# Kernel optimization log

Hardware: AMD Instinct MI355X
Metric: run time of the kernel (lower is better)

## Reference

```python
import jax, jax.numpy as jnp
from jax import lax
import numpy as np

B, N, C = 4, 2048, 64          # batch, num points, feature channels
M = 512                         # num centroids (FPS)
SAMPLES = (32, 64)              # neighbors per scale
RADII = (0.2, 0.4)              # ball radii per scale
MLPS = ((67, 64, 64, 128), (67, 128, 128, 256))  # in->hidden->out per scale (in = C + 3)


def setup_inputs() -> dict:
    key = jax.random.key(0)
    ks = jax.random.split(key, 16)
    inp = {
        "points": jax.random.uniform(ks[0], (B, 3, N), jnp.float32),   # unit cube
        "features": jax.random.normal(ks[1], (B, C, N), jnp.float32),
    }
    k = 2
    for s, dims in enumerate(MLPS):
        for l in range(3):
            cin, cout = dims[l], dims[l + 1]
            inp[f"w{s}_{l}"] = (jax.random.normal(ks[k], (cout, cin), jnp.float32)
                                * jnp.float32(1.0 / np.sqrt(cin)))
            inp[f"b{s}_{l}"] = jnp.zeros((cout,), jnp.float32)
            k += 1
    return inp


def fps(xyz, m):
    """Farthest point sampling. xyz: (B,N,3) -> indices (B,m) int32."""
    b, n, _ = xyz.shape
    big = jnp.asarray(1e10, xyz.dtype)

    def step(carry, _):
        dist, cur = carry                                   # (B,N), (B,)
        cur_pt = jnp.take_along_axis(xyz, cur[:, None, None], axis=1)  # (B,1,3)
        d2 = jnp.sum((xyz - cur_pt) ** 2, axis=-1)          # (B,N)
        dist = jnp.minimum(dist, d2)
        nxt = jnp.argmax(dist, axis=-1).astype(jnp.int32)
        return (dist, nxt), cur

    init = (jnp.full((b, n), big, xyz.dtype), jnp.zeros((b,), jnp.int32))
    _, idxs = lax.scan(step, init, None, length=m)          # (m,B)
    return idxs.T                                           # (B,m)


def ball_group(xyz, feat_t, cent, s, r):
    """Ball query + group gather. Returns (B,M,s,3+C) = [rel_xyz; features]."""
    n = xyz.shape[1]
    d2 = jnp.sum((cent[:, :, None, :] - xyz[:, None, :, :]) ** 2, axis=-1)  # (B,M,N)
    keys = jnp.where(d2 <= r * r, jnp.arange(n, dtype=jnp.int32), n)
    idx = jnp.sort(keys, axis=-1)[:, :, :s]                 # first s in-ball indices
    idx = jnp.where(idx < n, idx, idx[:, :, :1])            # pad with first valid
    gxyz = jax.vmap(lambda p, i: p[i])(xyz, idx) - cent[:, :, None, :]  # (B,M,s,3)
    gfeat = jax.vmap(lambda f, i: f[i])(feat_t, idx)        # (B,M,s,C)
    return jnp.concatenate([gxyz, gfeat], axis=-1)


def mlp_max(g, ws, bs):
    """Shared 1x1-conv MLP over (B,M,S,Cin), max over neighbor dim S."""
    x = g
    for w, b in zip(ws, bs):
        x = jax.nn.relu(jnp.einsum('bmsc,oc->bmso', x, w) + b)
    return jnp.max(x, axis=2)                               # (B,M,Cout)


def reference(points, features,
              w0_0, b0_0, w0_1, b0_1, w0_2, b0_2,
              w1_0, b1_0, w1_1, b1_1, w1_2, b1_2):
    xyz = jnp.transpose(points, (0, 2, 1))                  # (B,N,3)
    feat_t = jnp.transpose(features, (0, 2, 1))             # (B,N,C)
    idx = fps(xyz, M)                                       # (B,M)
    cent = jnp.take_along_axis(xyz, idx[:, :, None], axis=1)  # (B,M,3)
    Ws = [(w0_0, w0_1, w0_2), (w1_0, w1_1, w1_2)]
    Bs = [(b0_0, b0_1, b0_2), (b1_0, b1_1, b1_2)]
    outs = []
    for i, (s, r) in enumerate(zip(SAMPLES, RADII)):
        g = ball_group(xyz, feat_t, cent, s, r)             # (B,M,s,3+C)
        outs.append(mlp_max(g, Ws[i], Bs[i]))               # (B,M,Cout_i)
    feat = jnp.transpose(jnp.concatenate(outs, axis=-1), (0, 2, 1))  # (B,384,M)
    return jnp.transpose(cent, (0, 2, 1)), feat             # (B,3,M), (B,384,M)
```

## Files before the change

kernel.cpp:

```cpp
#include <hip/hip_runtime.h>

#define NPTS 2048
#define BATCH 4
#define CFEAT 64
#define MCENT 512

typedef float f4 __attribute__((ext_vector_type(4)));
typedef float f2 __attribute__((ext_vector_type(2)));
typedef short s8v __attribute__((ext_vector_type(8)));

__device__ __forceinline__ unsigned short f2bf(float x) {
    unsigned u = __float_as_uint(x);
    return (unsigned short)((u + 0x7fffu + ((u >> 16) & 1u)) >> 16);
}

template <int CTRL>
__device__ __forceinline__ float dpp_max_step(float v) {
    int t = __builtin_amdgcn_update_dpp(0, __float_as_int(v), CTRL, 0xf, 0xf, true);
    return fmaxf(v, __int_as_float(t));
}

__device__ __forceinline__ float readlane_f(float v, int l) {
    return __int_as_float(__builtin_amdgcn_readlane(__float_as_int(v), l));
}

template <int COUT, int CIN, int KPW, bool PERM>
__device__ void pack_seg(const float* w, unsigned short* dst, int start, int stride) {
    for (int i = start; i < COUT * KPW; i += stride) {
        int o = i / KPW, k = i - o * KPW;
        float v = 0.f;
        if (PERM) {
            if (k < 64) v = w[o * CIN + 3 + k];
            else if (k < 67) v = w[o * CIN + (k - 64)];
        } else {
            if (k < CIN) v = w[o * CIN + k];
        }
        dst[i] = f2bf(v);
    }
}

__global__ __launch_bounds__(256, 1) void fps_prep(
    const float* __restrict__ pts, const float* __restrict__ feats,
    const float* w00, const float* w01, const float* w02,
    const float* w10, const float* w11, const float* w12,
    float* cent, unsigned short* ftr, unsigned short* wp, float* out)
{
    const int tid = threadIdx.x;
    if (blockIdx.x >= 4) {
        const int stride = 64 * 256;
        const int start = (blockIdx.x - 4) * 256 + tid;
        for (int i = start; i < BATCH * NPTS * CFEAT; i += stride) {
            int c = i & 63, n = (i >> 6) & (NPTS - 1), b = i >> 17;
            ftr[i] = f2bf(feats[(b * CFEAT + c) * NPTS + n]);
        }
        pack_seg<64, 67, 96, true>(w00, wp + 0, start, stride);
        pack_seg<64, 64, 64, false>(w01, wp + 6144, start, stride);
        pack_seg<128, 64, 64, false>(w02, wp + 10240, start, stride);
        pack_seg<128, 67, 96, true>(w10, wp + 18432, start, stride);
        pack_seg<128, 128, 128, false>(w11, wp + 30720, start, stride);
        pack_seg<256, 128, 128, false>(w12, wp + 47104, start, stride);
        return;
    }
    const int b = blockIdx.x;
    const int lane = tid & 63, wv = tid >> 6;
    const float* px = pts + b * 3 * NPTS;
    const float* py = px + NPTS;
    const float* pz = py + NPTS;
    __shared__ __align__(16) float4 slotq[8 * 2];
    __shared__ __align__(16) float4 scent[MCENT];

    __builtin_amdgcn_s_setprio(3);

    const int base = wv * 512 + lane * 8;
    f2 rx[4], ry[4], rz[4], rd[4];
#pragma unroll
    for (int i = 0; i < 4; ++i) {
        rx[i] = *(const f2*)(px + base + 2 * i);
        ry[i] = *(const f2*)(py + base + 2 * i);
        rz[i] = *(const f2*)(pz + base + 2 * i);
        rd[i] = (f2){1e10f, 1e10f};
    }
    float cx = px[0], cy = py[0], cz = pz[0];
    int par = 0;
    for (int m = 0; m < MCENT; ++m) {
        if (tid == 0) scent[m] = make_float4(cx, cy, cz, 0.f);
        {
#pragma clang fp contract(off)
            f2 c2x = {cx, cx}, c2y = {cy, cy}, c2z = {cz, cz};
#pragma unroll
            for (int i = 0; i < 4; ++i) {
                f2 dx = rx[i] - c2x, dy = ry[i] - c2y, dz = rz[i] - c2z;
                f2 d2 = dx * dx + dy * dy;
                d2 = d2 + dz * dz;
                f2 old = rd[i];
                f2 nd;
                nd.x = fminf(old.x, d2.x);
                nd.y = fminf(old.y, d2.y);
                rd[i] = nd;
            }
        }
        float n0 = rd[0].x, n1 = rd[0].y, n2 = rd[1].x, n3 = rd[1].y;
        float n4 = rd[2].x, n5 = rd[2].y, n6 = rd[3].x, n7 = rd[3].y;
        float bv = fmaxf(fmaxf(fmaxf(n0, n1), fmaxf(n2, n3)),
                         fmaxf(fmaxf(n4, n5), fmaxf(n6, n7)));
        float ox = rx[3].y, oy = ry[3].y, oz = rz[3].y;
        {
            float ndv[8] = {n0, n1, n2, n3, n4, n5, n6, n7};
#pragma unroll
            for (int k = 6; k >= 0; --k) {
                bool t = (ndv[k] == bv);
                float nx = (k & 1) ? rx[k >> 1].y : rx[k >> 1].x;
                float ny = (k & 1) ? ry[k >> 1].y : ry[k >> 1].x;
                float nz = (k & 1) ? rz[k >> 1].y : rz[k >> 1].x;
                ox = t ? nx : ox; oy = t ? ny : oy; oz = t ? nz : oz;
            }
        }
        float v = bv;
        v = dpp_max_step<0x111>(v);
        v = dpp_max_step<0x112>(v);
        v = dpp_max_step<0x114>(v);
        v = dpp_max_step<0x118>(v);
        v = dpp_max_step<0x142>(v);
        v = dpp_max_step<0x143>(v);
        float wmax = readlane_f(v, 63);
        unsigned long long cand = __ballot(bv == wmax);
        int wl = __ffsll(cand) - 1;
        if (lane == wl) slotq[(par * 4 + wv) * 2] = make_float4(bv, ox, oy, oz);
        __syncthreads();
        float4 s0 = slotq[(par * 4 + 0) * 2];
        float4 s1 = slotq[(par * 4 + 1) * 2];
        float4 s2 = slotq[(par * 4 + 2) * 2];
        float4 s3 = slotq[(par * 4 + 3) * 2];
        float4 c01 = (s1.x > s0.x) ? s1 : s0;
        float4 c23 = (s3.x > s2.x) ? s3 : s2;
        float4 cc  = (c23.x > c01.x) ? c23 : c01;
        cx = cc.y; cy = cc.z; cz = cc.w;
        par ^= 1;
    }
    __syncthreads();
    float* outc = out + b * 3 * MCENT;
    for (int m = tid; m < MCENT; m += 256) {
        float4 c = scent[m];
        float* cw = cent + (b * MCENT + m) * 3;
        cw[0] = c.x; cw[1] = c.y; cw[2] = c.z;
        outc[m] = c.x; outc[MCENT + m] = c.y; outc[2 * MCENT + m] = c.z;
    }
}

template <int MT, int KSTEPS, int NTW>
__device__ __forceinline__ void layer_mm(const unsigned short* A, const unsigned short* __restrict__ Wg,
                                         const float* __restrict__ bias, int lane, int wv,
                                         f4 (&acc)[MT][NTW])
{
    constexpr int KP = KSTEPS * 32;
    const int r15 = lane & 15, g = lane >> 4;
#pragma unroll
    for (int nt = 0; nt < NTW; ++nt) {
        int n = (wv * NTW + nt) * 16 + r15;
        float bv = bias[n];
#pragma unroll
        for (int mt = 0; mt < MT; ++mt) acc[mt][nt] = (f4){bv, bv, bv, bv};
    }
#pragma unroll
    for (int ks = 0; ks < KSTEPS; ++ks) {
        s8v afr[MT];
#pragma unroll
        for (int mt = 0; mt < MT; ++mt) {
            int row = mt * 16 + r15;
            int byte = ((row * KP + ks * 32 + g * 8) * 2) ^ ((row & 7) << 4);
            afr[mt] = *(const s8v*)((const char*)A + byte);
        }
#pragma unroll
        for (int nt = 0; nt < NTW; ++nt) {
            int n = (wv * NTW + nt) * 16 + r15;
            s8v bfr = *(const s8v*)(Wg + n * KP + ks * 32 + g * 8);
#pragma unroll
            for (int mt = 0; mt < MT; ++mt)
                acc[mt][nt] = __builtin_amdgcn_mfma_f32_16x16x32_bf16(afr[mt], bfr, acc[mt][nt], 0, 0, 0);
        }
    }
}

template <int MT, int NTW, int CO>
__device__ __forceinline__ void store_lds(f4 (&acc)[MT][NTW], unsigned short* OUT, int lane, int wv) {
    const int r15 = lane & 15, g = lane >> 4;
#pragma unroll
    for (int mt = 0; mt < MT; ++mt)
#pragma unroll
        for (int nt = 0; nt < NTW; ++nt)
#pragma unroll
            for (int q = 0; q < 4; ++q) {
                int j = mt * 16 + g * 4 + q;
                int n = (wv * NTW + nt) * 16 + r15;
                float v = fmaxf(acc[mt][nt][q], 0.f);
                int byte = ((j * CO + n) * 2) ^ ((j & 7) << 4);
                *(unsigned short*)((char*)OUT + byte) = f2bf(v);
            }
}

template <int S_, int C1, int C2, int C3>
__device__ __forceinline__ void msg_body(int bm, char* smem,
    const float* __restrict__ pts, const unsigned short* __restrict__ ftr,
    const float* __restrict__ cent,
    const unsigned short* __restrict__ W0, const float* __restrict__ B0,
    const unsigned short* __restrict__ W1, const float* __restrict__ B1,
    const unsigned short* __restrict__ W2, const float* __restrict__ B2,
    float* __restrict__ outf, int ch_off, float rr)
{
    constexpr int MT = S_ / 16;
    constexpr int KS1 = C1 / 32, KS2 = C2 / 32;
    constexpr int NW1 = C1 / 64, NW2 = C2 / 64, NW3 = C3 / 64;
    constexpr int HA = (S_ * 96 > S_ * C2) ? S_ * 96 : S_ * C2;
    unsigned short* hA = (unsigned short*)smem;
    unsigned short* hB = hA + HA;
    int* nbr = (int*)(hB + S_ * C1);
    int* wtot = nbr + S_;
    const int tid = threadIdx.x, lane = tid & 63, wv = tid >> 6;
    const int b = bm >> 9, m = bm & (MCENT - 1);
    const float cx = cent[bm * 3], cy = cent[bm * 3 + 1], cz = cent[bm * 3 + 2];
    const float* px = pts + b * 3 * NPTS;
    const float* py = px + NPTS;
    const float* pz = py + NPTS;

    unsigned mask = 0; int cnt = 0;
    {
#pragma clang fp contract(off)
#pragma unroll
        for (int k = 0; k < 8; ++k) {
            int n = tid * 8 + k;
            float dx = cx - px[n], dy = cy - py[n], dz = cz - pz[n];
            float d2 = dx * dx + dy * dy;
            d2 = d2 + dz * dz;
            if (d2 <= rr) { mask |= 1u << k; ++cnt; }
        }
    }
    int inc = cnt;
#pragma unroll
    for (int off = 1; off < 64; off <<= 1) {
        int t = __shfl_up(inc, off);
        if (lane >= off) inc += t;
    }
    if (lane == 63) wtot[wv] = inc;
    __syncthreads();
    int base = 0, tot = 0;
#pragma unroll
    for (int w = 0; w < 4; ++w) { int t = wtot[w]; tot += t; if (w < wv) base += t; }
    int pos = base + inc - cnt;
#pragma unroll
    for (int k = 0; k < 8; ++k) {
        if ((mask >> k) & 1) {
            if (pos < S_) nbr[pos] = tid * 8 + k;
            ++pos;
        }
    }
    __syncthreads();
    const int first = nbr[0];

    for (int e = tid; e < S_ * 8; e += 256) {
        int j = e >> 3, c8 = e & 7;
        int p = (j < tot) ? nbr[j] : first;
        s8v v = *(const s8v*)(ftr + (b * NPTS + p) * 64 + c8 * 8);
        int byte = ((j * 96 + c8 * 8) * 2) ^ ((j & 7) << 4);
        *(s8v*)((char*)hA + byte) = v;
    }
    for (int e = tid; e < S_ * 4; e += 256) {
        int j = e >> 2, q = e & 3;
        int p = (j < tot) ? nbr[j] : first;
        s8v v = {0, 0, 0, 0, 0, 0, 0, 0};
        if (q == 0) {
            v[0] = (short)f2bf(px[p] - cx);
            v[1] = (short)f2bf(py[p] - cy);
            v[2] = (short)f2bf(pz[p] - cz);
        }
        int byte = ((j * 96 + 64 + q * 8) * 2) ^ ((j & 7) << 4);
        *(s8v*)((char*)hA + byte) = v;
    }
    __syncthreads();

    {
        f4 acc[MT][NW1];
        layer_mm<MT, 3, NW1>(hA, W0, B0, lane, wv, acc);
        store_lds<MT, NW1, C1>(acc, hB, lane, wv);
    }
    __syncthreads();
    {
        f4 acc[MT][NW2];
        layer_mm<MT, KS1, NW2>(hB, W1, B1, lane, wv, acc);
        store_lds<MT, NW2, C2>(acc, hA, lane, wv);
    }
    __syncthreads();
    {
        f4 acc[MT][NW3];
        layer_mm<MT, KS2, NW3>(hA, W2, B2, lane, wv, acc);
        const int r15 = lane & 15;
        float* dst = outf + b * 384 * MCENT + ch_off * MCENT + m;
#pragma unroll
        for (int nt = 0; nt < NW3; ++nt) {
            float mv = -1e30f;
#pragma unroll
            for (int mt = 0; mt < MT; ++mt)
#pragma unroll
                for (int q = 0; q < 4; ++q) mv = fmaxf(mv, acc[mt][nt][q]);
            mv = fmaxf(mv, __shfl_xor(mv, 16));
            mv = fmaxf(mv, __shfl_xor(mv, 32));
            float v = fmaxf(mv, 0.f);
            if (lane < 16) dst[((wv * NW3 + nt) * 16 + r15) * MCENT] = v;
        }
    }
}

__global__ __launch_bounds__(256) void msg_both(
    const float* __restrict__ pts, const unsigned short* __restrict__ ftr,
    const float* __restrict__ cent, const unsigned short* __restrict__ wp,
    const float* __restrict__ b00, const float* __restrict__ b01, const float* __restrict__ b02,
    const float* __restrict__ b10, const float* __restrict__ b11, const float* __restrict__ b12,
    float* __restrict__ outf, float rr0, float rr1)
{
    extern __shared__ __align__(16) char smem[];
    if (blockIdx.x < BATCH * MCENT)
        msg_body<32, 64, 64, 128>(blockIdx.x, smem, pts, ftr, cent,
                                  wp + 0, b00, wp + 6144, b01, wp + 10240, b02, outf, 0, rr0);
    else
        msg_body<64, 128, 128, 256>(blockIdx.x - BATCH * MCENT, smem, pts, ftr, cent,
                                    wp + 18432, b10, wp + 30720, b11, wp + 47104, b12, outf, 128, rr1);
}

extern "C" void kernel_launch(void* const* d_in, const int* in_sizes, int n_in,
                              void* d_out, int out_size, void* d_ws, size_t ws_size,
                              hipStream_t stream) {
    const float* pts  = (const float*)d_in[0];
    const float* feats = (const float*)d_in[1];
    const float* w00 = (const float*)d_in[2];  const float* b00 = (const float*)d_in[3];
    const float* w01 = (const float*)d_in[4];  const float* b01 = (const float*)d_in[5];
    const float* w02 = (const float*)d_in[6];  const float* b02 = (const float*)d_in[7];
    const float* w10 = (const float*)d_in[8];  const float* b10 = (const float*)d_in[9];
    const float* w11 = (const float*)d_in[10]; const float* b11 = (const float*)d_in[11];
    const float* w12 = (const float*)d_in[12]; const float* b12 = (const float*)d_in[13];
    float* out = (float*)d_out;
    char* ws = (char*)d_ws;
    float* cent = (float*)ws;
    unsigned short* ftr = (unsigned short*)(ws + 24576);
    unsigned short* wp  = (unsigned short*)(ws + 24576 + 1048576);

    hipLaunchKernelGGL(fps_prep, dim3(68), dim3(256), 0, stream,
                       pts, feats, w00, w01, w02, w10, w11, w12, cent, ftr, wp, out);
    float* outf = out + BATCH * 3 * MCENT;
    const float RR0 = (float)(0.2 * 0.2);
    const float RR1 = (float)(0.4 * 0.4);
    hipLaunchKernelGGL(msg_both, dim3(2 * BATCH * MCENT), dim3(256), 33040, stream,
                       pts, ftr, cent, wp, b00, b01, b02, b10, b11, b12, outf, RR0, RR1);
}
```

Before: 291.3 us.

## Run FPS for all four batches in one 1024-thread block

Merges the four per-batch FPS blocks into a single 1024-thread block where each group of four waves handles one batch, with per-batch shared slot and centroid arrays. The prep blocks become 1024 threads wide and the grid shrinks to 65 blocks. One block-wide __syncthreads per iteration now couples all four batches, so every batch waits on the slowest wave. Putting all four batches on one CU also means they share its issue bandwidth, which likely lengthens the serial FPS chain.

```diff
diff --git a/kernel.cpp b/kernel.cpp
--- a/kernel.cpp
+++ b/kernel.cpp
@@ -39,16 +39,16 @@
     }
 }
 
-__global__ __launch_bounds__(256, 1) void fps_prep(
+__global__ __launch_bounds__(1024, 1) void fps_prep(
     const float* __restrict__ pts, const float* __restrict__ feats,
     const float* w00, const float* w01, const float* w02,
     const float* w10, const float* w11, const float* w12,
     float* cent, unsigned short* ftr, unsigned short* wp, float* out)
 {
     const int tid = threadIdx.x;
-    if (blockIdx.x >= 4) {
-        const int stride = 64 * 256;
-        const int start = (blockIdx.x - 4) * 256 + tid;
+    if (blockIdx.x >= 1) {
+        const int stride = 64 * 1024;
+        const int start = (blockIdx.x - 1) * 1024 + tid;
         for (int i = start; i < BATCH * NPTS * CFEAT; i += stride) {
             int c = i & 63, n = (i >> 6) & (NPTS - 1), b = i >> 17;
             ftr[i] = f2bf(feats[(b * CFEAT + c) * NPTS + n]);
@@ -61,17 +61,17 @@
         pack_seg<256, 128, 128, false>(w12, wp + 47104, start, stride);
         return;
     }
-    const int b = blockIdx.x;
     const int lane = tid & 63, wv = tid >> 6;
-    const float* px = pts + b * 3 * NPTS;
+    const int c = wv >> 2, w4 = wv & 3;
+    const float* px = pts + c * 3 * NPTS;
     const float* py = px + NPTS;
     const float* pz = py + NPTS;
-    __shared__ __align__(16) float4 slotq[8 * 2];
-    __shared__ __align__(16) float4 scent[MCENT];
+    __shared__ __align__(16) float4 scent[BATCH][MCENT];
+    __shared__ __align__(16) float4 slotq[BATCH][2][8];
 
     __builtin_amdgcn_s_setprio(3);
 
-    const int base = wv * 512 + lane * 8;
+    const int base = w4 * 512 + lane * 8;
     f2 rx[4], ry[4], rz[4], rd[4];
 #pragma unroll
     for (int i = 0; i < 4; ++i) {
@@ -83,7 +83,7 @@
     float cx = px[0], cy = py[0], cz = pz[0];
     int par = 0;
     for (int m = 0; m < MCENT; ++m) {
-        if (tid == 0) scent[m] = make_float4(cx, cy, cz, 0.f);
+        if (lane == 0 && w4 == 0) scent[c][m] = make_float4(cx, cy, cz, 0.f);
         {
 #pragma clang fp contract(off)
             f2 c2x = {cx, cx}, c2y = {cy, cy}, c2z = {cz, cz};
@@ -125,12 +125,12 @@
         float wmax = readlane_f(v, 63);
         unsigned long long cand = __ballot(bv == wmax);
         int wl = __ffsll(cand) - 1;
-        if (lane == wl) slotq[(par * 4 + wv) * 2] = make_float4(bv, ox, oy, oz);
+        if (lane == wl) slotq[c][par][w4 * 2] = make_float4(bv, ox, oy, oz);
         __syncthreads();
-        float4 s0 = slotq[(par * 4 + 0) * 2];
-        float4 s1 = slotq[(par * 4 + 1) * 2];
-        float4 s2 = slotq[(par * 4 + 2) * 2];
-        float4 s3 = slotq[(par * 4 + 3) * 2];
+        float4 s0 = slotq[c][par][0];
+        float4 s1 = slotq[c][par][2];
+        float4 s2 = slotq[c][par][4];
+        float4 s3 = slotq[c][par][6];
         float4 c01 = (s1.x > s0.x) ? s1 : s0;
         float4 c23 = (s3.x > s2.x) ? s3 : s2;
         float4 cc  = (c23.x > c01.x) ? c23 : c01;
@@ -138,12 +138,13 @@
         par ^= 1;
     }
     __syncthreads();
-    float* outc = out + b * 3 * MCENT;
-    for (int m = tid; m < MCENT; m += 256) {
-        float4 c = scent[m];
-        float* cw = cent + (b * MCENT + m) * 3;
-        cw[0] = c.x; cw[1] = c.y; cw[2] = c.z;
-        outc[m] = c.x; outc[MCENT + m] = c.y; outc[2 * MCENT + m] = c.z;
+    for (int i = tid; i < BATCH * MCENT; i += 1024) {
+        int c2 = i >> 9, m = i & (MCENT - 1);
+        float4 cc = scent[c2][m];
+        float* cw = cent + (c2 * MCENT + m) * 3;
+        cw[0] = cc.x; cw[1] = cc.y; cw[2] = cc.z;
+        float* outc = out + c2 * 3 * MCENT;
+        outc[m] = cc.x; outc[MCENT + m] = cc.y; outc[2 * MCENT + m] = cc.z;
     }
 }
 
@@ -342,7 +343,7 @@
     unsigned short* ftr = (unsigned short*)(ws + 24576);
     unsigned short* wp  = (unsigned short*)(ws + 24576 + 1048576);
 
-    hipLaunchKernelGGL(fps_prep, dim3(68), dim3(256), 0, stream,
+    hipLaunchKernelGGL(fps_prep, dim3(65), dim3(1024), 0, stream,
                        pts, feats, w00, w01, w02, w10, w11, w12, cent, ftr, wp, out);
     float* outf = out + BATCH * 3 * MCENT;
     const float RR0 = (float)(0.2 * 0.2);
```

Result: slower. 561.7 us (+92.8%).
